# Optimization experiments

Hardware: AMD Instinct MI355X
Metric: run time of the kernel (lower is better)

The kernel has to match this reference:

```python
import jax, jax.numpy as jnp
import numpy as np

B, T, D = 8, 2048, 1024


def setup_inputs() -> dict:
    key = jax.random.key(0)
    ks = jax.random.split(key, 9)
    s = 1.0 / np.sqrt(D)
    return {
        "e": jax.random.normal(ks[0], (B, T, D), jnp.float32),
        "residual": jax.random.normal(ks[1], (B, T, D), jnp.float32),
        "Wq_w": jax.random.normal(ks[2], (D, D), jnp.float32) * s,
        "Wq_b": jax.random.normal(ks[3], (D,), jnp.float32) * s,
        "Wk_w": jax.random.normal(ks[4], (D, D), jnp.float32) * s,
        "Wk_b": jax.random.normal(ks[5], (D,), jnp.float32) * s,
        "Wv_w": jax.random.normal(ks[6], (D, D), jnp.float32) * s,
        "Wv_b": jax.random.normal(ks[7], (D,), jnp.float32) * s,
        "v_table": jax.random.normal(ks[8], (T, 1), jnp.float32),
    }


def reference(e, residual, Wq_w, Wq_b, Wk_w, Wk_b, Wv_w, Wv_b, v_table):
    T_ = e.shape[1]
    # relative position index: pos[i,j] = max(i - j, 0)
    pos = jnp.arange(T_)
    rel = jnp.maximum(pos[:, None] - pos[None, :], 0)          # (T, T) int
    pos_embd = v_table[rel, 0]                                 # (T, T) gather from Embedding(length, 1)

    # torch Linear: x @ W.T + b
    Q = e @ Wq_w.T + Wq_b                                      # (B, T, D)
    K = residual @ Wk_w.T + Wk_b                               # (B, T, D)
    V = e @ Wv_w.T + Wv_b                                      # (B, T, D)

    # Q @ K^T  (torch: Q @ Wk(residual).transpose(-2,-1))
    scores = jnp.einsum('btd,bsd->bts', Q, K)                  # (B, T, T)
    # einsum('BeT,Tt->BTt', K^T, pos_embd) == sum_e K[B,T,e] * pos_embd[T,t]
    scores = scores + K.sum(-1)[:, :, None] * pos_embd[None]   # (B, T, T)

    # causal mask via tril (zeros strictly-upper entries); NO softmax in this variant
    scores = scores * jnp.tril(jnp.ones((T_, T_), scores.dtype))
    return scores @ V                                          # (B, T, D)
```

## Files before the change

kernel.cpp:

```cpp
#include <hip/hip_runtime.h>

typedef unsigned short u16;
typedef __attribute__((ext_vector_type(8))) short bf16x8;
typedef __attribute__((ext_vector_type(8))) unsigned short u16x8;
typedef __attribute__((ext_vector_type(4))) float f32x4;

static __device__ __forceinline__ u16 f2bf(float f) {
  unsigned u = __float_as_uint(f);
  u += 0x7FFFu + ((u >> 16) & 1u);
  return (u16)(u >> 16);
}
static __device__ __forceinline__ float bf2f(u16 h) {
  return __uint_as_float(((unsigned)h) << 16);
}

__global__ __launch_bounds__(256) void conv_big(const float* __restrict__ e,
                                                const float* __restrict__ res,
                                                u16* __restrict__ eb, u16* __restrict__ rb) {
  int i = blockIdx.x * 256 + threadIdx.x;
  const float* in = blockIdx.z ? res : e;
  u16* out = blockIdx.z ? rb : eb;
  const float4* p = (const float4*)in + (size_t)i * 2;
  float4 a = p[0], b = p[1];
  u16x8 r;
  r[0] = f2bf(a.x); r[1] = f2bf(a.y); r[2] = f2bf(a.z); r[3] = f2bf(a.w);
  r[4] = f2bf(b.x); r[5] = f2bf(b.y); r[6] = f2bf(b.z); r[7] = f2bf(b.w);
  ((u16x8*)out)[i] = r;
}
__global__ __launch_bounds__(256) void conv_w(const float* __restrict__ w0,
                                              const float* __restrict__ w1,
                                              const float* __restrict__ w2,
                                              u16* __restrict__ o0, u16* __restrict__ o1,
                                              u16* __restrict__ o2) {
  int i = blockIdx.x * 256 + threadIdx.x;
  const float* in = blockIdx.z == 0 ? w0 : (blockIdx.z == 1 ? w1 : w2);
  u16* out = blockIdx.z == 0 ? o0 : (blockIdx.z == 1 ? o1 : o2);
  const float4* p = (const float4*)in + (size_t)i * 2;
  float4 a = p[0], b = p[1];
  u16x8 r;
  r[0] = f2bf(a.x); r[1] = f2bf(a.y); r[2] = f2bf(a.z); r[3] = f2bf(a.w);
  r[4] = f2bf(b.x); r[5] = f2bf(b.y); r[6] = f2bf(b.z); r[7] = f2bf(b.w);
  ((u16x8*)out)[i] = r;
}

__global__ __launch_bounds__(256) void ksum_kernel(const u16* __restrict__ K,
                                                   float* __restrict__ out) {
  int row = blockIdx.x * 4 + (threadIdx.x >> 6);
  int lane = threadIdx.x & 63;
  const u16x8* p = (const u16x8*)(K + (size_t)row * 1024);
  float s = 0.f;
#pragma unroll
  for (int it = 0; it < 2; ++it) {
    u16x8 v = p[lane + it * 64];
#pragma unroll
    for (int j = 0; j < 8; ++j) s += bf2f(v[j]);
  }
#pragma unroll
  for (int off = 32; off >= 1; off >>= 1) s += __shfl_down(s, off);
  if (lane == 0) out[row] = s;
}

enum { M_BIASN = 0, M_BIASM = 1, M_SCORES = 2, M_OUT = 3 };

template <int MODE>
static __device__ __forceinline__ void core128(
    const u16* __restrict__ Ab, int lda, const u16* __restrict__ Bb, int ldb,
    char* smem, int m0, int n0, int nk, void* __restrict__ Cbase, int ldc,
    const float* __restrict__ bias, const float* __restrict__ ksb,
    const float* __restrict__ vtab) {
  const int tid = threadIdx.x;
  const int lane = tid & 63;
  const int wid = tid >> 6;
  const int wm = wid >> 1, wn = wid & 1;

  char* As = smem;
  char* Bs = smem + 16384;

  const int rbase_st = tid >> 3;
  const int gcol = ((tid & 7) << 4) ^ ((rbase_st & 7) << 4);

  const int aoff = (wm * 64 + (lane & 15)) * 128;
  const int boff = (wn * 64 + (lane & 15)) * 128;
  const int c0 = ((0 * 4 + (lane >> 4)) ^ (lane & 7)) << 4;
  const int c1 = ((1 * 4 + (lane >> 4)) ^ (lane & 7)) << 4;

  f32x4 acc[4][4];
#pragma unroll
  for (int m = 0; m < 4; ++m)
#pragma unroll
    for (int n = 0; n < 4; ++n) acc[m][n] = (f32x4){0.f, 0.f, 0.f, 0.f};

  for (int kt = 0; kt < nk; ++kt) {
    const int k0 = kt * 64;
#pragma unroll
    for (int i = 0; i < 4; ++i) {
      const char* ga = (const char*)(Ab + (size_t)(m0 + i * 32 + rbase_st) * lda + k0) + gcol;
      __builtin_amdgcn_global_load_lds(
          (const __attribute__((address_space(1))) void*)ga,
          (__attribute__((address_space(3))) void*)(As + i * 4096 + wid * 1024), 16, 0, 0);
    }
#pragma unroll
    for (int i = 0; i < 4; ++i) {
      const char* gb = (const char*)(Bb + (size_t)(n0 + i * 32 + rbase_st) * ldb + k0) + gcol;
      __builtin_amdgcn_global_load_lds(
          (const __attribute__((address_space(1))) void*)gb,
          (__attribute__((address_space(3))) void*)(Bs + i * 4096 + wid * 1024), 16, 0, 0);
    }
    __syncthreads();
#pragma unroll
    for (int ks = 0; ks < 2; ++ks) {
      const int cks = ks ? c1 : c0;
      bf16x8 af[4], bfv[4];
#pragma unroll
      for (int m = 0; m < 4; ++m) af[m] = *(const bf16x8*)(As + aoff + m * 2048 + cks);
#pragma unroll
      for (int n = 0; n < 4; ++n) bfv[n] = *(const bf16x8*)(Bs + boff + n * 2048 + cks);
#pragma unroll
      for (int m = 0; m < 4; ++m)
#pragma unroll
        for (int n = 0; n < 4; ++n)
          acc[m][n] = __builtin_amdgcn_mfma_f32_16x16x32_bf16(af[m], bfv[n], acc[m][n], 0, 0, 0);
    }
    __syncthreads();
  }

  u16* C16 = (u16*)Cbase;
  float* Cf = (float*)Cbase;
#pragma unroll
  for (int m = 0; m < 4; ++m) {
#pragma unroll
    for (int n = 0; n < 4; ++n) {
      const int rb = m0 + wm * 64 + m * 16 + ((lane >> 4) << 2);
      const int c = n0 + wn * 64 + n * 16 + (lane & 15);
#pragma unroll
      for (int j = 0; j < 4; ++j) {
        const int r = rb + j;
        float v = acc[m][n][j];
        if (MODE == M_BIASN) {
          v += bias[c];
          C16[(size_t)r * ldc + c] = f2bf(v);
        } else if (MODE == M_BIASM) {
          v += bias[r];
          C16[(size_t)r * ldc + c] = f2bf(v);
        } else if (MODE == M_SCORES) {
          if (c <= r) v += ksb[r] * vtab[r - c];
          else v = 0.f;
          C16[(size_t)r * ldc + c] = f2bf(v);
        } else {
          Cf[(size_t)r * ldc + c] = v;
        }
      }
    }
  }
}

__global__ __launch_bounds__(256, 4) void k_qk_proj(
    const u16* eb, const u16* rb, const u16* Wq, const u16* Wk,
    const float* bq, const float* bk, u16* Q, u16* K) {
  const int l = blockIdx.x;
  const int xcd = l & 7;
  const int idx = l >> 3;
  const bool isK = idx >= 128;
  const int j = idx & 127;
  const int gy = xcd * 16 + (j >> 3);
  const int gx = j & 7;
  const u16* A = isK ? rb : eb;
  const u16* B = isK ? Wk : Wq;
  const float* bias = isK ? bk : bq;
  u16* C = isK ? K : Q;
  __shared__ char smem[32768];
  core128<M_BIASN>(A, 1024, B, 1024, smem, gy * 128, gx * 128, 16,
                   C, 1024, bias, nullptr, nullptr);
}
__global__ __launch_bounds__(256, 4) void k_v_proj(
    const u16* Wv, const u16* eb, u16* VT, const float* bv) {
  const int l = blockIdx.x;
  const int xcd = l & 7;
  const int idx = l >> 3;
  const int gxt = xcd * 16 + (idx >> 3);
  const int gyd = idx & 7;
  __shared__ char smem[32768];
  core128<M_BIASM>(Wv, 1024, eb, 1024, smem, gyd * 128, gxt * 128, 16,
                   VT, 16384, bv, nullptr, nullptr);
}
__global__ __launch_bounds__(256, 4) void k_scores(
    const u16* Q, const u16* K, u16* S, const float* ksum, const float* vtab) {
  const int l = blockIdx.x;
  const int z = l & 7;
  const int h = l >> 3;
  int gy = 0;
#pragma unroll
  for (int q = 1; q < 16; ++q) if (q * (q + 1) / 2 <= h) gy = q;
  const int gx = h - gy * (gy + 1) / 2;
  __shared__ char smem[32768];
  core128<M_SCORES>(Q + (size_t)z * 2048 * 1024, 1024,
                    K + (size_t)z * 2048 * 1024, 1024, smem,
                    gy * 128, gx * 128, 16,
                    S + (size_t)z * 2048 * 2048, 2048,
                    nullptr, ksum + (size_t)z * 2048, vtab);
}
__global__ __launch_bounds__(256, 4) void k_out(
    const u16* S, const u16* VT, float* O) {
  const int l = blockIdx.x;
  const int z = l & 7;
  const int idx = l >> 3;
  const int gy = 15 - (idx >> 3);
  const int gx = idx & 7;
  const int nk = (gy + 1) * 2;
  __shared__ char smem[32768];
  core128<M_OUT>(S + (size_t)z * 2048 * 2048, 2048,
                 VT + (size_t)z * 2048, 16384, smem,
                 gy * 128, gx * 128, nk,
                 O + (size_t)z * 2048 * 1024, 1024,
                 nullptr, nullptr, nullptr);
}

extern "C" void kernel_launch(void* const* d_in, const int* in_sizes, int n_in,
                              void* d_out, int out_size, void* d_ws, size_t ws_size,
                              hipStream_t stream) {
  (void)in_sizes; (void)n_in; (void)out_size; (void)ws_size;
  const float* e    = (const float*)d_in[0];
  const float* res  = (const float*)d_in[1];
  const float* Wq_w = (const float*)d_in[2];
  const float* Wq_b = (const float*)d_in[3];
  const float* Wk_w = (const float*)d_in[4];
  const float* Wk_b = (const float*)d_in[5];
  const float* Wv_w = (const float*)d_in[6];
  const float* Wv_b = (const float*)d_in[7];
  const float* vtab = (const float*)d_in[8];

  char* ws = (char*)d_ws;
  const size_t SZ = 33554432;
  u16* ebf = (u16*)(ws);
  u16* rbf = (u16*)(ws + SZ);
  u16* Qb  = (u16*)(ws + 2 * SZ);
  u16* Kb  = (u16*)(ws + 3 * SZ);
  u16* VT  = (u16*)(ws + 4 * SZ);
  u16* Wqb = (u16*)(ws + 5 * SZ);
  u16* Wkb = (u16*)(ws + 5 * SZ + 2097152);
  u16* Wvb = (u16*)(ws + 5 * SZ + 2 * 2097152);
  float* ksum = (float*)(ws + 5 * SZ + 3 * 2097152);
  u16* scores = (u16*)(ws);

  conv_big<<<dim3(8192, 1, 2), 256, 0, stream>>>(e, res, ebf, rbf);
  conv_w<<<dim3(512, 1, 3), 256, 0, stream>>>(Wq_w, Wk_w, Wv_w, Wqb, Wkb, Wvb);

  k_qk_proj<<<dim3(2048, 1, 1), 256, 0, stream>>>(ebf, rbf, Wqb, Wkb, Wq_b, Wk_b, Qb, Kb);
  k_v_proj<<<dim3(1024, 1, 1), 256, 0, stream>>>(Wvb, ebf, VT, Wv_b);

  ksum_kernel<<<4096, 256, 0, stream>>>(Kb, ksum);

  k_scores<<<dim3(1088, 1, 1), 256, 0, stream>>>(Qb, Kb, scores, ksum, vtab);

  k_out<<<dim3(1024, 1, 1), 256, 0, stream>>>(scores, VT, (float*)d_out);
}
```

Before: 256.6 us.

## Use 256x256 tiles with multi-stage async LDS pipeline for projection GEMMs

Replaces the 128x128 projection GEMM kernels (Q/K and V) with a 512-thread, 256x256-tile engine. It uses a 9-slot LDS ring buffer of 16 KB half-tiles, filled via direct global-to-LDS loads and issued several stages ahead, with explicit vmcnt waits, barriers, sched barriers and setprio around the MFMA clusters. The aim is to raise arithmetic intensity and hide global load latency behind matrix math. In exchange it uses 144 KB of LDS per block, which lowers occupancy and adds grid-size and tail-wave risk. The scores and output kernels are unchanged.

```diff
diff --git a/kernel.cpp b/kernel.cpp
--- a/kernel.cpp
+++ b/kernel.cpp
@@ -4,6 +4,11 @@
 typedef __attribute__((ext_vector_type(8))) short bf16x8;
 typedef __attribute__((ext_vector_type(8))) unsigned short u16x8;
 typedef __attribute__((ext_vector_type(4))) float f32x4;
+
+#define AS1 __attribute__((address_space(1)))
+#define AS3 __attribute__((address_space(3)))
+#define SBAR __builtin_amdgcn_sched_barrier(0)
+#define LG0  asm volatile("s_waitcnt lgkmcnt(0)" ::: "memory")
 
 static __device__ __forceinline__ u16 f2bf(float f) {
   unsigned u = __float_as_uint(f);
@@ -62,6 +67,156 @@
 
 enum { M_BIASN = 0, M_BIASM = 1, M_SCORES = 2, M_OUT = 3 };
 
+#define MM16(mb, af_, bf_)                                                      \
+  { _Pragma("unroll") for (int m_ = 0; m_ < 4; ++m_)                            \
+      _Pragma("unroll") for (int n_ = 0; n_ < 4; ++n_)                          \
+        acc[(mb) + m_][n_] = __builtin_amdgcn_mfma_f32_16x16x32_bf16(           \
+            af_[m_], bf_[n_], acc[(mb) + m_][n_], 0, 0, 0); }
+
+#define ISSUE(ui_, slot_)                                                       \
+  {                                                                             \
+    const int p_ = (ui_) & 3;                                                   \
+    const u16* src_ = (p_ < 2) ? A : B;                                         \
+    const int ld_ = (p_ < 2) ? lda : ldb;                                       \
+    const int r0_ = ((p_ < 2) ? m0 : n0) + (p_ & 1) * 128;                      \
+    const int k0_ = ((ui_) >> 2) * 64;                                          \
+    char* dst_ = smem + (slot_) * 16384;                                        \
+    _Pragma("unroll") for (int h_ = 0; h_ < 2; ++h_) {                          \
+      const char* g_ = (const char*)(src_ + (size_t)(r0_ + h_ * 64 + strow) * ld_ + k0_) + gcol; \
+      __builtin_amdgcn_global_load_lds((const AS1 void*)g_,                     \
+          (AS3 void*)(dst_ + h_ * 8192 + sdst), 16, 0, 0);                      \
+    }                                                                           \
+  }
+
+template <int MODE>
+static __device__ __forceinline__ void engine256(
+    const u16* __restrict__ A, int lda, const u16* __restrict__ B, int ldb,
+    char* smem, int m0, int n0, int nk, void* __restrict__ Cbase, int ldc,
+    const float* __restrict__ bias) {
+  const int tid = threadIdx.x;
+  const int lane = tid & 63;
+  const int wid = tid >> 6;
+  const int wm = wid >> 2, wn = wid & 3;
+
+  const int strow = tid >> 3;
+  const int gcol = ((tid & 7) << 4) ^ ((strow & 7) << 4);
+  const int sdst = tid << 4;
+
+  const int roff = (lane & 15) * 128;
+  const int c0 = ((0 + (lane >> 4)) ^ (lane & 7)) << 4;
+  const int c1 = ((4 + (lane >> 4)) ^ (lane & 7)) << 4;
+
+  f32x4 acc[8][4];
+#pragma unroll
+  for (int m = 0; m < 8; ++m)
+#pragma unroll
+    for (int n = 0; n < 4; ++n) acc[m][n] = (f32x4){0.f, 0.f, 0.f, 0.f};
+
+#pragma unroll
+  for (int u = 0; u < 5; ++u) ISSUE(u, u);
+  int ui = 5, si = 5;
+  int sbase = 0;
+  const int lim = 4 * nk;
+
+  for (int t = 0; t < nk; ++t) {
+    int sA = sbase + wm; if (sA >= 9) sA -= 9;
+    int sB = sbase + 2 + (wn >> 1); if (sB >= 9) sB -= 9;
+    const char* Au = smem + sA * 16384;
+    const char* Bu = smem + sB * 16384 + (wn & 1) * 8192;
+    bf16x8 afa[4], afb[4], bfa[4], bfb[4];
+
+    if (t + 1 == nk) { asm volatile("s_waitcnt vmcnt(0)" ::: "memory"); }
+    else             { asm volatile("s_waitcnt vmcnt(2)" ::: "memory"); }
+    __builtin_amdgcn_s_barrier();
+    if (ui < lim) { ISSUE(ui, si); ++ui; if (++si == 9) si = 0; }
+    if (ui < lim) { ISSUE(ui, si); ++ui; if (++si == 9) si = 0; }
+#pragma unroll
+    for (int f = 0; f < 4; ++f) afa[f] = *(const bf16x8*)(Au + f * 2048 + roff + c0);
+#pragma unroll
+    for (int f = 0; f < 4; ++f) bfa[f] = *(const bf16x8*)(Bu + f * 2048 + roff + c0);
+    LG0; SBAR;
+    __builtin_amdgcn_s_setprio(1);
+    MM16(0, afa, bfa);
+    __builtin_amdgcn_s_setprio(0);
+
+    __builtin_amdgcn_s_barrier();
+    if (ui < lim) { ISSUE(ui, si); ++ui; if (++si == 9) si = 0; }
+    if (ui < lim) { ISSUE(ui, si); ++ui; if (++si == 9) si = 0; }
+#pragma unroll
+    for (int f = 0; f < 4; ++f) afb[f] = *(const bf16x8*)(Au + 8192 + f * 2048 + roff + c0);
+    LG0; SBAR;
+    __builtin_amdgcn_s_setprio(1);
+    MM16(4, afb, bfa);
+    __builtin_amdgcn_s_setprio(0);
+
+    __builtin_amdgcn_s_barrier();
+#pragma unroll
+    for (int f = 0; f < 4; ++f) afa[f] = *(const bf16x8*)(Au + f * 2048 + roff + c1);
+#pragma unroll
+    for (int f = 0; f < 4; ++f) bfb[f] = *(const bf16x8*)(Bu + f * 2048 + roff + c1);
+    LG0; SBAR;
+    __builtin_amdgcn_s_setprio(1);
+    MM16(0, afa, bfb);
+    __builtin_amdgcn_s_setprio(0);
+
+    __builtin_amdgcn_s_barrier();
+#pragma unroll
+    for (int f = 0; f < 4; ++f) afb[f] = *(const bf16x8*)(Au + 8192 + f * 2048 + roff + c1);
+    LG0; SBAR;
+    __builtin_amdgcn_s_setprio(1);
+    MM16(4, afb, bfb);
+    __builtin_amdgcn_s_setprio(0);
+
+    sbase += 4; if (sbase >= 9) sbase -= 9;
+  }
+
+  u16* C16 = (u16*)Cbase;
+#pragma unroll
+  for (int m = 0; m < 8; ++m) {
+#pragma unroll
+    for (int n = 0; n < 4; ++n) {
+      const int rb = m0 + wm * 128 + m * 16 + ((lane >> 4) << 2);
+      const int c = n0 + wn * 64 + n * 16 + (lane & 15);
+#pragma unroll
+      for (int j = 0; j < 4; ++j) {
+        const int r = rb + j;
+        float v = acc[m][n][j];
+        v += (MODE == M_BIASN) ? bias[c] : bias[r];
+        C16[(size_t)r * ldc + c] = f2bf(v);
+      }
+    }
+  }
+}
+
+__global__ __launch_bounds__(512, 2) void k_qk_proj(
+    const u16* eb, const u16* rb, const u16* Wq, const u16* Wk,
+    const float* bq, const float* bk, u16* Q, u16* K) {
+  const int l = blockIdx.x;
+  const int xcd = l & 7;
+  const int idx = l >> 3;
+  const bool isK = idx >= 32;
+  const int j = idx & 31;
+  const int gy = xcd * 8 + (j >> 2);
+  const int gx = j & 3;
+  const u16* A = isK ? rb : eb;
+  const u16* B = isK ? Wk : Wq;
+  const float* bias = isK ? bk : bq;
+  u16* C = isK ? K : Q;
+  __shared__ char smem[147456];
+  engine256<M_BIASN>(A, 1024, B, 1024, smem, gy * 256, gx * 256, 16, C, 1024, bias);
+}
+__global__ __launch_bounds__(512, 2) void k_v_proj(
+    const u16* Wv, const u16* eb, u16* VT, const float* bv) {
+  const int l = blockIdx.x;
+  const int xcd = l & 7;
+  const int idx = l >> 3;
+  const int gxt = xcd * 8 + (idx >> 2);
+  const int gyd = idx & 3;
+  __shared__ char smem[147456];
+  engine256<M_BIASM>(Wv, 1024, eb, 1024, smem, gyd * 256, gxt * 256, 16,
+                     VT, 16384, bv);
+}
+
 template <int MODE>
 static __device__ __forceinline__ void core128(
     const u16* __restrict__ Ab, int lda, const u16* __restrict__ Bb, int ldb,
@@ -96,15 +251,13 @@
     for (int i = 0; i < 4; ++i) {
       const char* ga = (const char*)(Ab + (size_t)(m0 + i * 32 + rbase_st) * lda + k0) + gcol;
       __builtin_amdgcn_global_load_lds(
-          (const __attribute__((address_space(1))) void*)ga,
-          (__attribute__((address_space(3))) void*)(As + i * 4096 + wid * 1024), 16, 0, 0);
+          (const AS1 void*)ga, (AS3 void*)(As + i * 4096 + wid * 1024), 16, 0, 0);
     }
 #pragma unroll
     for (int i = 0; i < 4; ++i) {
       const char* gb = (const char*)(Bb + (size_t)(n0 + i * 32 + rbase_st) * ldb + k0) + gcol;
       __builtin_amdgcn_global_load_lds(
-          (const __attribute__((address_space(1))) void*)gb,
-          (__attribute__((address_space(3))) void*)(Bs + i * 4096 + wid * 1024), 16, 0, 0);
+          (const AS1 void*)gb, (AS3 void*)(Bs + i * 4096 + wid * 1024), 16, 0, 0);
     }
     __syncthreads();
 #pragma unroll
@@ -136,13 +289,7 @@
       for (int j = 0; j < 4; ++j) {
         const int r = rb + j;
         float v = acc[m][n][j];
-        if (MODE == M_BIASN) {
-          v += bias[c];
-          C16[(size_t)r * ldc + c] = f2bf(v);
-        } else if (MODE == M_BIASM) {
-          v += bias[r];
-          C16[(size_t)r * ldc + c] = f2bf(v);
-        } else if (MODE == M_SCORES) {
+        if (MODE == M_SCORES) {
           if (c <= r) v += ksb[r] * vtab[r - c];
           else v = 0.f;
           C16[(size_t)r * ldc + c] = f2bf(v);
@@ -154,35 +301,6 @@
   }
 }
 
-__global__ __launch_bounds__(256, 4) void k_qk_proj(
-    const u16* eb, const u16* rb, const u16* Wq, const u16* Wk,
-    const float* bq, const float* bk, u16* Q, u16* K) {
-  const int l = blockIdx.x;
-  const int xcd = l & 7;
-  const int idx = l >> 3;
-  const bool isK = idx >= 128;
-  const int j = idx & 127;
-  const int gy = xcd * 16 + (j >> 3);
-  const int gx = j & 7;
-  const u16* A = isK ? rb : eb;
-  const u16* B = isK ? Wk : Wq;
-  const float* bias = isK ? bk : bq;
-  u16* C = isK ? K : Q;
-  __shared__ char smem[32768];
-  core128<M_BIASN>(A, 1024, B, 1024, smem, gy * 128, gx * 128, 16,
-                   C, 1024, bias, nullptr, nullptr);
-}
-__global__ __launch_bounds__(256, 4) void k_v_proj(
-    const u16* Wv, const u16* eb, u16* VT, const float* bv) {
-  const int l = blockIdx.x;
-  const int xcd = l & 7;
-  const int idx = l >> 3;
-  const int gxt = xcd * 16 + (idx >> 3);
-  const int gyd = idx & 7;
-  __shared__ char smem[32768];
-  core128<M_BIASM>(Wv, 1024, eb, 1024, smem, gyd * 128, gxt * 128, 16,
-                   VT, 16384, bv, nullptr, nullptr);
-}
 __global__ __launch_bounds__(256, 4) void k_scores(
     const u16* Q, const u16* K, u16* S, const float* ksum, const float* vtab) {
   const int l = blockIdx.x;
@@ -245,8 +363,8 @@
   conv_big<<<dim3(8192, 1, 2), 256, 0, stream>>>(e, res, ebf, rbf);
   conv_w<<<dim3(512, 1, 3), 256, 0, stream>>>(Wq_w, Wk_w, Wv_w, Wqb, Wkb, Wvb);
 
-  k_qk_proj<<<dim3(2048, 1, 1), 256, 0, stream>>>(ebf, rbf, Wqb, Wkb, Wq_b, Wk_b, Qb, Kb);
-  k_v_proj<<<dim3(1024, 1, 1), 256, 0, stream>>>(Wvb, ebf, VT, Wv_b);
+  k_qk_proj<<<dim3(512, 1, 1), 512, 0, stream>>>(ebf, rbf, Wqb, Wkb, Wq_b, Wk_b, Qb, Kb);
+  k_v_proj<<<dim3(256, 1, 1), 512, 0, stream>>>(Wvb, ebf, VT, Wv_b);
 
   ksum_kernel<<<4096, 256, 0, stream>>>(Kb, ksum);
 
```

Result: slower. 270.7 us (+5.5%).
